# Performance work log

Hardware: AMD Instinct MI355X
Metric: run time of the kernel (lower is better)

## Reference

```python
import jax, jax.numpy as jnp
import numpy as np
from jax import lax

P_COARSE, P_FINE = 8, 4
EMBED_DIM = 128


def _patchify(x, p):
    # torch unfold(kernel=p, stride=p) then transpose: [B, Hp*Wp, C*p*p]
    B, C, H, W = x.shape
    Hp, Wp = H // p, W // p
    t = x.reshape(B, C, Hp, p, Wp, p).transpose(0, 2, 4, 1, 3, 5)
    return t.reshape(B, Hp * Wp, C * p * p), Hp, Wp


def _edge_map(x):
    gray = x.mean(axis=1, keepdims=True)
    kx = jnp.array([[-1., 0., 1.], [-2., 0., 2.], [-1., 0., 1.]], gray.dtype)[None, None]
    ky = jnp.array([[-1., -2., -1.], [0., 0., 0.], [1., 2., 1.]], gray.dtype)[None, None]
    pad = [(1, 1), (1, 1)]
    sx = lax.conv_general_dilated(gray, kx, (1, 1), pad)
    sy = lax.conv_general_dilated(gray, ky, (1, 1), pad)
    e = jnp.sqrt(sx * sx + sy * sy)
    B, _, H, W = e.shape
    # avg_pool2d(4, stride=4)
    return e.reshape(B, 1, H // 4, 4, W // 4, 4).mean(axis=(3, 5))


def _compact(tok, m):
    # stream-compact masked rows to the front, zero-pad the rest (pad_sequence semantics, padded to full Nf)
    Nf, D = tok.shape
    pos = jnp.cumsum(m) - 1
    pos = jnp.where(m, pos, Nf)  # unmasked rows go to overflow slot
    out = jnp.zeros((Nf + 1, D), tok.dtype).at[pos].set(tok)
    return out[:Nf]


def setup_inputs() -> dict:
    key = jax.random.key(0)
    ks = jax.random.split(key, 6)
    D = EMBED_DIM
    pd_c = 1 * P_COARSE * P_COARSE
    pd_f = 1 * P_FINE * P_FINE
    return {
        "x": jax.random.normal(ks[0], (8, 1, 512, 512), jnp.float32),
        "w_coarse": jax.random.normal(ks[1], (pd_c, D), jnp.float32) / np.sqrt(pd_c),
        "b_coarse": jnp.zeros((D,), jnp.float32),
        "w_fine": jax.random.normal(ks[2], (pd_f, D), jnp.float32) / np.sqrt(pd_f),
        "b_fine": jnp.zeros((D,), jnp.float32),
        "type_emb": jax.random.normal(ks[3], (2, D), jnp.float32) * 0.02,
    }


def reference(x, w_coarse, b_coarse, w_fine, b_fine, type_emb):
    B = x.shape[0]
    # coarse branch
    pc, Hc, Wc = _patchify(x, P_COARSE)
    coarse = pc @ w_coarse + b_coarse + type_emb[0]  # [B, Nc, D]
    # edge-driven mask
    edges = _edge_map(x)  # [B,1,He,We]
    mask = edges > edges.mean(axis=(2, 3), keepdims=True)
    # fine branch
    pf, Hf, Wf = _patchify(x, P_FINE)
    fine = pf @ w_fine + b_fine  # [B, Nf, D]
    # nearest upsample mask to (Hf, Wf): integer factor repeat
    m = mask[:, 0]
    m = jnp.repeat(jnp.repeat(m, Hf // m.shape[1], axis=1), Wf // m.shape[2], axis=2)
    mask_flat = m.reshape(B, -1)  # [B, Nf]
    fine_c = jax.vmap(_compact)(fine, mask_flat) + type_emb[1]
    tokens = jnp.concatenate([coarse, fine_c], axis=1)
    return tokens, mask_flat
```

## Files before the change

### kernel.cpp

```cpp
#include <hip/hip_runtime.h>

#define IMH 512
#define IMW 512
#define BATCH 8
#define NTOK 20480
#define NC 4096
#define NF 16384
#define ED 128

__global__ __launch_bounds__(256) void k_edge(const float* __restrict__ x,
                                              double* __restrict__ edges,
                                              double* __restrict__ tsum) {
    __shared__ float esm[66][68];
    __shared__ double dred[4];
    int blk = blockIdx.x;
    int t = threadIdx.x;
    int lane = t & 63, wid = t >> 6;
    int b = blk >> 6;
    int tile = blk & 63;
    int ty0 = (tile >> 3) * 64;
    int tx0 = (tile & 7) * 64;
    const float* img = x + (size_t)b * (IMH * IMW);
    for (int idx = t; idx < 66 * 66; idx += 256) {
        int r = idx / 66, c = idx - r * 66;
        int gy = ty0 - 1 + r, gx = tx0 - 1 + c;
        float v = 0.f;
        if (gy >= 0 && gy < IMH && gx >= 0 && gx < IMW) v = img[gy * IMW + gx];
        esm[r][c] = v;
    }
    __syncthreads();
    int cy = t >> 4, cx = t & 15;
    double acc = 0.0;
    #pragma unroll
    for (int dy = 0; dy < 4; ++dy) {
        int py = cy * 4 + dy + 1;
        #pragma unroll
        for (int dx = 0; dx < 4; ++dx) {
            int px = cx * 4 + dx + 1;
            double a00 = (double)esm[py - 1][px - 1];
            double a01 = (double)esm[py - 1][px];
            double a02 = (double)esm[py - 1][px + 1];
            double a10 = (double)esm[py][px - 1];
            double a12 = (double)esm[py][px + 1];
            double a20 = (double)esm[py + 1][px - 1];
            double a21 = (double)esm[py + 1][px];
            double a22 = (double)esm[py + 1][px + 1];
            double sx = (a02 + 2.0 * a12 + a22) - (a00 + 2.0 * a10 + a20);
            double sy = (a20 + 2.0 * a21 + a22) - (a00 + 2.0 * a01 + a02);
            acc += sqrt(sx * sx + sy * sy);
        }
    }
    double cell = acc * (1.0 / 16.0);
    int gy = (ty0 >> 2) + cy;
    int gx = (tx0 >> 2) + cx;
    edges[((size_t)b << 14) + gy * 128 + gx] = cell;
    double sc = cell;
    #pragma unroll
    for (int off = 32; off > 0; off >>= 1) sc += __shfl_xor(sc, off);
    if (lane == 0) dred[wid] = sc;
    __syncthreads();
    if (t == 0) tsum[b * 64 + tile] = dred[0] + dred[1] + dred[2] + dred[3];
}

__global__ __launch_bounds__(1024) void k_scan(const double* __restrict__ edges,
                                               const double* __restrict__ tsum,
                                               int* __restrict__ pos,
                                               int* __restrict__ Karr,
                                               float* __restrict__ mask_out) {
    int b = blockIdx.x;
    int t = threadIdx.x;
    int lane = t & 63, wid = t >> 6;
    __shared__ int wcnt[16];
    const double* ts = tsum + b * 64;
    double total = 0.0;
    #pragma unroll
    for (int j = 0; j < 64; ++j) total += ts[j];
    double mean = total * (1.0 / 16384.0);

    const double* e = edges + ((size_t)b << 14);
    double v[16];
    #pragma unroll
    for (int j = 0; j < 8; ++j) {
        double2 dv = *(const double2*)&e[t * 16 + j * 2];
        v[2 * j] = dv.x; v[2 * j + 1] = dv.y;
    }
    int m[16], cnt = 0;
    #pragma unroll
    for (int j = 0; j < 16; ++j) { m[j] = (v[j] > mean) ? 1 : 0; cnt += m[j]; }
    int incl = cnt;
    #pragma unroll
    for (int off = 1; off < 64; off <<= 1) {
        int up = __shfl_up(incl, off);
        if (lane >= off) incl += up;
    }
    if (lane == 63) wcnt[wid] = incl;
    __syncthreads();
    int woff = 0, Ktot = 0;
    #pragma unroll
    for (int w = 0; w < 16; ++w) { int c = wcnt[w]; Ktot += c; if (w < wid) woff += c; }
    int run = woff + incl - cnt;
    float mf[16]; int pv[16];
    #pragma unroll
    for (int j = 0; j < 16; ++j) {
        pv[j] = m[j] ? run : -1;
        run += m[j];
        mf[j] = m[j] ? 1.0f : 0.0f;
    }
    float* mb = mask_out + ((size_t)b << 14) + t * 16;
    int* pb = pos + ((size_t)b << 14) + t * 16;
    #pragma unroll
    for (int q = 0; q < 4; ++q) {
        *(float4*)&mb[q * 4] = make_float4(mf[4 * q], mf[4 * q + 1], mf[4 * q + 2], mf[4 * q + 3]);
        *(int4*)&pb[q * 4] = make_int4(pv[4 * q], pv[4 * q + 1], pv[4 * q + 2], pv[4 * q + 3]);
    }
    if (t == 0) Karr[b] = Ktot;
}

__global__ __launch_bounds__(256) void k_mega(const float* __restrict__ x,
                                              const float* __restrict__ wc,
                                              const float* __restrict__ bc,
                                              const float* __restrict__ wfp,
                                              const float* __restrict__ bfp,
                                              const float* __restrict__ temb,
                                              const int* __restrict__ pos,
                                              const int* __restrict__ Karr,
                                              float* __restrict__ out) {
    __shared__ float smx[4][256];
    int blk = blockIdx.x;
    int t = threadIdx.x;
    int lane = t & 63;
    int b = blk >> 7;
    int r128 = blk & 127;

    {
        int pblk = r128 * 32;
        int wv = __builtin_amdgcn_readfirstlane(t >> 6);
        int h = wv & 1;
        int p0 = pblk + (wv >> 1) * 16;
        int d = h * 64 + lane;
        float wcol[64];
        #pragma unroll
        for (int k = 0; k < 64; ++k) wcol[k] = wc[k * ED + d];
        float base = bc[d] + temb[d];
        const float* img = x + ((size_t)b * IMH + (p0 >> 6) * 8) * IMW + (p0 & 63) * 8;
        float* dst = out + ((size_t)b * NTOK + p0) * ED + d;
        #pragma unroll
        for (int p = 0; p < 16; ++p) {
            const float* pimg = img + p * 8;
            float acc = base;
            #pragma unroll
            for (int r = 0; r < 8; ++r) {
                const float* rp = pimg + r * IMW;
                acc += rp[0] * wcol[r * 8 + 0] + rp[1] * wcol[r * 8 + 1]
                     + rp[2] * wcol[r * 8 + 2] + rp[3] * wcol[r * 8 + 3]
                     + rp[4] * wcol[r * 8 + 4] + rp[5] * wcol[r * 8 + 5]
                     + rp[6] * wcol[r * 8 + 6] + rp[7] * wcol[r * 8 + 7];
            }
            dst[(size_t)p * ED] = acc;
        }
    }
    asm volatile("" ::: "memory");

    int d4 = t & 31;
    int g = t >> 5;
    float4 wcol[16];
    #pragma unroll
    for (int k = 0; k < 16; ++k) wcol[k] = *(const float4*)&wfp[k * ED + d4 * 4];
    float4 fill = *(const float4*)&temb[ED + d4 * 4];
    float4 bse = *(const float4*)&bfp[d4 * 4];
    float4 fbase = make_float4(bse.x + fill.x, bse.y + fill.y, bse.z + fill.z, bse.w + fill.w);
    int K = Karr[b];
    const int* posb = pos + ((size_t)b << 14);
    float* tok = out + ((size_t)b * NTOK + NC) * ED;

    #pragma unroll
    for (int u = 0; u < 2; ++u) {
        int i0 = (r128 * 2 + u) * 64;
        int hf = i0 >> 7;
        int wf0 = i0 & 127;
        const float* img = x + ((size_t)b * IMH + hf * 4) * IMW + wf0 * 4;
        __syncthreads();
        {
            int r = t >> 6, c4 = t & 63;
            *(float4*)&smx[r][c4 * 4] = *(const float4*)&img[r * IMW + c4 * 4];
        }
        __syncthreads();
        #pragma unroll
        for (int pp = 0; pp < 8; ++pp) {
            int p = g + pp * 8;
            int i = i0 + p;
            int ps = posb[i];
            if (ps >= 0) {
                float4 acc = fbase;
                #pragma unroll
                for (int r = 0; r < 4; ++r) {
                    float4 vv = *(const float4*)&smx[r][p * 4];
                    acc.x += vv.x * wcol[4 * r].x + vv.y * wcol[4 * r + 1].x + vv.z * wcol[4 * r + 2].x + vv.w * wcol[4 * r + 3].x;
                    acc.y += vv.x * wcol[4 * r].y + vv.y * wcol[4 * r + 1].y + vv.z * wcol[4 * r + 2].y + vv.w * wcol[4 * r + 3].y;
                    acc.z += vv.x * wcol[4 * r].z + vv.y * wcol[4 * r + 1].z + vv.z * wcol[4 * r + 2].z + vv.w * wcol[4 * r + 3].z;
                    acc.w += vv.x * wcol[4 * r].w + vv.y * wcol[4 * r + 1].w + vv.z * wcol[4 * r + 2].w + vv.w * wcol[4 * r + 3].w;
                }
                *(float4*)(tok + ((size_t)ps * 32 + d4) * 4) = acc;
            }
            if (i >= K) {
                *(float4*)(tok + ((size_t)i * 32 + d4) * 4) = fill;
            }
        }
    }
}

extern "C" void kernel_launch(void* const* d_in, const int* in_sizes, int n_in,
                              void* d_out, int out_size, void* d_ws, size_t ws_size,
                              hipStream_t stream) {
    const float* x    = (const float*)d_in[0];
    const float* wc   = (const float*)d_in[1];
    const float* bc   = (const float*)d_in[2];
    const float* wfp  = (const float*)d_in[3];
    const float* bfp  = (const float*)d_in[4];
    const float* temb = (const float*)d_in[5];
    float* out = (float*)d_out;

    char* wsb = (char*)d_ws;
    double* edges = (double*)wsb;
    double* tsum  = (double*)(wsb + (size_t)BATCH * NF * 8);
    int* pos  = (int*)(wsb + (size_t)BATCH * NF * 8 + 4096);
    int* Karr = (int*)(wsb + (size_t)BATCH * NF * 8 + 4096 + (size_t)BATCH * NF * 4);
    float* mask_out = out + (size_t)BATCH * NTOK * ED;

    k_edge<<<dim3(512), 256, 0, stream>>>(x, edges, tsum);
    k_scan<<<dim3(BATCH), 1024, 0, stream>>>(edges, tsum, pos, Karr, mask_out);
    k_mega<<<dim3(1024), 256, 0, stream>>>(x, wc, bc, wfp, bfp, temb, pos, Karr, out);
}
```

Before: 54.68 us.

## Move coarse projection into edge kernel and restructure fine projection kernel

The coarse patch projection moves out of the final kernel and into the edge-map kernel as extra blocks. It no longer depends on the mask, so it can run before the serial scan instead of after it. The fine projection becomes its own kernel: each thread computes one output column for 16 patches and reads pixels straight from global memory instead of staging them in shared memory. This shortens the critical path after the scan, at the cost of uncoalesced-looking scalar image reads and a larger first kernel.

```diff
diff --git a/kernel.cpp b/kernel.cpp
--- a/kernel.cpp
+++ b/kernel.cpp
@@ -8,132 +8,21 @@
 #define NF 16384
 #define ED 128
 
-__global__ __launch_bounds__(256) void k_edge(const float* __restrict__ x,
-                                              double* __restrict__ edges,
-                                              double* __restrict__ tsum) {
+__global__ __launch_bounds__(256) void k1_edge_coarse(const float* __restrict__ x,
+                                                      const float* __restrict__ wc,
+                                                      const float* __restrict__ bc,
+                                                      const float* __restrict__ temb,
+                                                      float* __restrict__ out,
+                                                      double* __restrict__ edges,
+                                                      double* __restrict__ tsum) {
     __shared__ float esm[66][68];
     __shared__ double dred[4];
     int blk = blockIdx.x;
     int t = threadIdx.x;
     int lane = t & 63, wid = t >> 6;
-    int b = blk >> 6;
-    int tile = blk & 63;
-    int ty0 = (tile >> 3) * 64;
-    int tx0 = (tile & 7) * 64;
-    const float* img = x + (size_t)b * (IMH * IMW);
-    for (int idx = t; idx < 66 * 66; idx += 256) {
-        int r = idx / 66, c = idx - r * 66;
-        int gy = ty0 - 1 + r, gx = tx0 - 1 + c;
-        float v = 0.f;
-        if (gy >= 0 && gy < IMH && gx >= 0 && gx < IMW) v = img[gy * IMW + gx];
-        esm[r][c] = v;
-    }
-    __syncthreads();
-    int cy = t >> 4, cx = t & 15;
-    double acc = 0.0;
-    #pragma unroll
-    for (int dy = 0; dy < 4; ++dy) {
-        int py = cy * 4 + dy + 1;
-        #pragma unroll
-        for (int dx = 0; dx < 4; ++dx) {
-            int px = cx * 4 + dx + 1;
-            double a00 = (double)esm[py - 1][px - 1];
-            double a01 = (double)esm[py - 1][px];
-            double a02 = (double)esm[py - 1][px + 1];
-            double a10 = (double)esm[py][px - 1];
-            double a12 = (double)esm[py][px + 1];
-            double a20 = (double)esm[py + 1][px - 1];
-            double a21 = (double)esm[py + 1][px];
-            double a22 = (double)esm[py + 1][px + 1];
-            double sx = (a02 + 2.0 * a12 + a22) - (a00 + 2.0 * a10 + a20);
-            double sy = (a20 + 2.0 * a21 + a22) - (a00 + 2.0 * a01 + a02);
-            acc += sqrt(sx * sx + sy * sy);
-        }
-    }
-    double cell = acc * (1.0 / 16.0);
-    int gy = (ty0 >> 2) + cy;
-    int gx = (tx0 >> 2) + cx;
-    edges[((size_t)b << 14) + gy * 128 + gx] = cell;
-    double sc = cell;
-    #pragma unroll
-    for (int off = 32; off > 0; off >>= 1) sc += __shfl_xor(sc, off);
-    if (lane == 0) dred[wid] = sc;
-    __syncthreads();
-    if (t == 0) tsum[b * 64 + tile] = dred[0] + dred[1] + dred[2] + dred[3];
-}
-
-__global__ __launch_bounds__(1024) void k_scan(const double* __restrict__ edges,
-                                               const double* __restrict__ tsum,
-                                               int* __restrict__ pos,
-                                               int* __restrict__ Karr,
-                                               float* __restrict__ mask_out) {
-    int b = blockIdx.x;
-    int t = threadIdx.x;
-    int lane = t & 63, wid = t >> 6;
-    __shared__ int wcnt[16];
-    const double* ts = tsum + b * 64;
-    double total = 0.0;
-    #pragma unroll
-    for (int j = 0; j < 64; ++j) total += ts[j];
-    double mean = total * (1.0 / 16384.0);
-
-    const double* e = edges + ((size_t)b << 14);
-    double v[16];
-    #pragma unroll
-    for (int j = 0; j < 8; ++j) {
-        double2 dv = *(const double2*)&e[t * 16 + j * 2];
-        v[2 * j] = dv.x; v[2 * j + 1] = dv.y;
-    }
-    int m[16], cnt = 0;
-    #pragma unroll
-    for (int j = 0; j < 16; ++j) { m[j] = (v[j] > mean) ? 1 : 0; cnt += m[j]; }
-    int incl = cnt;
-    #pragma unroll
-    for (int off = 1; off < 64; off <<= 1) {
-        int up = __shfl_up(incl, off);
-        if (lane >= off) incl += up;
-    }
-    if (lane == 63) wcnt[wid] = incl;
-    __syncthreads();
-    int woff = 0, Ktot = 0;
-    #pragma unroll
-    for (int w = 0; w < 16; ++w) { int c = wcnt[w]; Ktot += c; if (w < wid) woff += c; }
-    int run = woff + incl - cnt;
-    float mf[16]; int pv[16];
-    #pragma unroll
-    for (int j = 0; j < 16; ++j) {
-        pv[j] = m[j] ? run : -1;
-        run += m[j];
-        mf[j] = m[j] ? 1.0f : 0.0f;
-    }
-    float* mb = mask_out + ((size_t)b << 14) + t * 16;
-    int* pb = pos + ((size_t)b << 14) + t * 16;
-    #pragma unroll
-    for (int q = 0; q < 4; ++q) {
-        *(float4*)&mb[q * 4] = make_float4(mf[4 * q], mf[4 * q + 1], mf[4 * q + 2], mf[4 * q + 3]);
-        *(int4*)&pb[q * 4] = make_int4(pv[4 * q], pv[4 * q + 1], pv[4 * q + 2], pv[4 * q + 3]);
-    }
-    if (t == 0) Karr[b] = Ktot;
-}
-
-__global__ __launch_bounds__(256) void k_mega(const float* __restrict__ x,
-                                              const float* __restrict__ wc,
-                                              const float* __restrict__ bc,
-                                              const float* __restrict__ wfp,
-                                              const float* __restrict__ bfp,
-                                              const float* __restrict__ temb,
-                                              const int* __restrict__ pos,
-                                              const int* __restrict__ Karr,
-                                              float* __restrict__ out) {
-    __shared__ float smx[4][256];
-    int blk = blockIdx.x;
-    int t = threadIdx.x;
-    int lane = t & 63;
-    int b = blk >> 7;
-    int r128 = blk & 127;
-
-    {
-        int pblk = r128 * 32;
+    if (blk < 1024) {
+        int b = blk >> 7;
+        int pblk = (blk & 127) * 32;
         int wv = __builtin_amdgcn_readfirstlane(t >> 6);
         int h = wv & 1;
         int p0 = pblk + (wv >> 1) * 16;
@@ -158,53 +47,151 @@
             }
             dst[(size_t)p * ED] = acc;
         }
-    }
-    asm volatile("" ::: "memory");
-
-    int d4 = t & 31;
-    int g = t >> 5;
-    float4 wcol[16];
-    #pragma unroll
-    for (int k = 0; k < 16; ++k) wcol[k] = *(const float4*)&wfp[k * ED + d4 * 4];
-    float4 fill = *(const float4*)&temb[ED + d4 * 4];
-    float4 bse = *(const float4*)&bfp[d4 * 4];
-    float4 fbase = make_float4(bse.x + fill.x, bse.y + fill.y, bse.z + fill.z, bse.w + fill.w);
+    } else {
+        int blk2 = blk - 1024;
+        int b = blk2 >> 6;
+        int tile = blk2 & 63;
+        int ty0 = (tile >> 3) * 64;
+        int tx0 = (tile & 7) * 64;
+        const float* img = x + (size_t)b * (IMH * IMW);
+        for (int idx = t; idx < 66 * 66; idx += 256) {
+            int r = idx / 66, c = idx - r * 66;
+            int gy = ty0 - 1 + r, gx = tx0 - 1 + c;
+            float v = 0.f;
+            if (gy >= 0 && gy < IMH && gx >= 0 && gx < IMW) v = img[gy * IMW + gx];
+            esm[r][c] = v;
+        }
+        __syncthreads();
+        int cy = t >> 4, cx = t & 15;
+        double acc = 0.0;
+        #pragma unroll
+        for (int dy = 0; dy < 4; ++dy) {
+            int py = cy * 4 + dy + 1;
+            #pragma unroll
+            for (int dx = 0; dx < 4; ++dx) {
+                int px = cx * 4 + dx + 1;
+                double a00 = (double)esm[py - 1][px - 1];
+                double a01 = (double)esm[py - 1][px];
+                double a02 = (double)esm[py - 1][px + 1];
+                double a10 = (double)esm[py][px - 1];
+                double a12 = (double)esm[py][px + 1];
+                double a20 = (double)esm[py + 1][px - 1];
+                double a21 = (double)esm[py + 1][px];
+                double a22 = (double)esm[py + 1][px + 1];
+                double sx = (a02 + 2.0 * a12 + a22) - (a00 + 2.0 * a10 + a20);
+                double sy = (a20 + 2.0 * a21 + a22) - (a00 + 2.0 * a01 + a02);
+                acc += sqrt(sx * sx + sy * sy);
+            }
+        }
+        double cell = acc * (1.0 / 16.0);
+        int gy = (ty0 >> 2) + cy;
+        int gx = (tx0 >> 2) + cx;
+        edges[((size_t)b << 14) + gy * 128 + gx] = cell;
+        double sc = cell;
+        #pragma unroll
+        for (int off = 32; off > 0; off >>= 1) sc += __shfl_xor(sc, off);
+        if (lane == 0) dred[wid] = sc;
+        __syncthreads();
+        if (t == 0) tsum[b * 64 + tile] = dred[0] + dred[1] + dred[2] + dred[3];
+    }
+}
+
+__global__ __launch_bounds__(1024) void k_scan(const double* __restrict__ edges,
+                                               const double* __restrict__ tsum,
+                                               int* __restrict__ pos,
+                                               int* __restrict__ Karr,
+                                               float* __restrict__ mask_out) {
+    int b = blockIdx.x;
+    int t = threadIdx.x;
+    int lane = t & 63, wid = t >> 6;
+    __shared__ int wcnt[16];
+    const double* ts = tsum + b * 64;
+    double total = 0.0;
+    #pragma unroll
+    for (int j = 0; j < 64; ++j) total += ts[j];
+    double mean = total * (1.0 / 16384.0);
+
+    const double* e = edges + ((size_t)b << 14);
+    double v[16];
+    #pragma unroll
+    for (int j = 0; j < 8; ++j) {
+        double2 dv = *(const double2*)&e[t * 16 + j * 2];
+        v[2 * j] = dv.x; v[2 * j + 1] = dv.y;
+    }
+    int m[16], cnt = 0;
+    #pragma unroll
+    for (int j = 0; j < 16; ++j) { m[j] = (v[j] > mean) ? 1 : 0; cnt += m[j]; }
+    int incl = cnt;
+    #pragma unroll
+    for (int off = 1; off < 64; off <<= 1) {
+        int up = __shfl_up(incl, off);
+        if (lane >= off) incl += up;
+    }
+    if (lane == 63) wcnt[wid] = incl;
+    __syncthreads();
+    int woff = 0, Ktot = 0;
+    #pragma unroll
+    for (int w = 0; w < 16; ++w) { int c = wcnt[w]; Ktot += c; if (w < wid) woff += c; }
+    int run = woff + incl - cnt;
+    float mf[16]; int pv[16];
+    #pragma unroll
+    for (int j = 0; j < 16; ++j) {
+        pv[j] = m[j] ? run : -1;
+        run += m[j];
+        mf[j] = m[j] ? 1.0f : 0.0f;
+    }
+    float* mb = mask_out + ((size_t)b << 14) + t * 16;
+    int* pb = pos + ((size_t)b << 14) + t * 16;
+    #pragma unroll
+    for (int q = 0; q < 4; ++q) {
+        *(float4*)&mb[q * 4] = make_float4(mf[4 * q], mf[4 * q + 1], mf[4 * q + 2], mf[4 * q + 3]);
+        *(int4*)&pb[q * 4] = make_int4(pv[4 * q], pv[4 * q + 1], pv[4 * q + 2], pv[4 * q + 3]);
+    }
+    if (t == 0) Karr[b] = Ktot;
+}
+
+__global__ __launch_bounds__(256) void k_fine(const float* __restrict__ x,
+                                              const float* __restrict__ wfp,
+                                              const float* __restrict__ bfp,
+                                              const float* __restrict__ temb,
+                                              const int* __restrict__ pos,
+                                              const int* __restrict__ Karr,
+                                              float* __restrict__ out) {
+    int b = blockIdx.y;
+    int t = threadIdx.x;
+    int lane = t & 63;
+    int wv = __builtin_amdgcn_readfirstlane(t >> 6);
+    int h = wv & 1;
+    int p0 = blockIdx.x * 32 + (wv >> 1) * 16;
+    int d = h * 64 + lane;
+    float wcol[16];
+    #pragma unroll
+    for (int k = 0; k < 16; ++k) wcol[k] = wfp[k * ED + d];
+    float fill = temb[ED + d];
+    float fbase = bfp[d] + fill;
     int K = Karr[b];
     const int* posb = pos + ((size_t)b << 14);
+    int hf = p0 >> 7;
+    int wf0 = p0 & 127;
+    const float* img = x + ((size_t)b * IMH + hf * 4) * IMW + wf0 * 4;
     float* tok = out + ((size_t)b * NTOK + NC) * ED;
-
-    #pragma unroll
-    for (int u = 0; u < 2; ++u) {
-        int i0 = (r128 * 2 + u) * 64;
-        int hf = i0 >> 7;
-        int wf0 = i0 & 127;
-        const float* img = x + ((size_t)b * IMH + hf * 4) * IMW + wf0 * 4;
-        __syncthreads();
-        {
-            int r = t >> 6, c4 = t & 63;
-            *(float4*)&smx[r][c4 * 4] = *(const float4*)&img[r * IMW + c4 * 4];
-        }
-        __syncthreads();
-        #pragma unroll
-        for (int pp = 0; pp < 8; ++pp) {
-            int p = g + pp * 8;
-            int i = i0 + p;
-            int ps = posb[i];
-            if (ps >= 0) {
-                float4 acc = fbase;
-                #pragma unroll
-                for (int r = 0; r < 4; ++r) {
-                    float4 vv = *(const float4*)&smx[r][p * 4];
-                    acc.x += vv.x * wcol[4 * r].x + vv.y * wcol[4 * r + 1].x + vv.z * wcol[4 * r + 2].x + vv.w * wcol[4 * r + 3].x;
-                    acc.y += vv.x * wcol[4 * r].y + vv.y * wcol[4 * r + 1].y + vv.z * wcol[4 * r + 2].y + vv.w * wcol[4 * r + 3].y;
-                    acc.z += vv.x * wcol[4 * r].z + vv.y * wcol[4 * r + 1].z + vv.z * wcol[4 * r + 2].z + vv.w * wcol[4 * r + 3].z;
-                    acc.w += vv.x * wcol[4 * r].w + vv.y * wcol[4 * r + 1].w + vv.z * wcol[4 * r + 2].w + vv.w * wcol[4 * r + 3].w;
-                }
-                *(float4*)(tok + ((size_t)ps * 32 + d4) * 4) = acc;
-            }
-            if (i >= K) {
-                *(float4*)(tok + ((size_t)i * 32 + d4) * 4) = fill;
-            }
+    #pragma unroll
+    for (int p = 0; p < 16; ++p) {
+        int i = p0 + p;
+        int ps = posb[i];
+        const float* pimg = img + p * 4;
+        float acc = fbase;
+        #pragma unroll
+        for (int r = 0; r < 4; ++r) {
+            const float* rp = pimg + r * IMW;
+            acc += rp[0] * wcol[4 * r + 0] + rp[1] * wcol[4 * r + 1]
+                 + rp[2] * wcol[4 * r + 2] + rp[3] * wcol[4 * r + 3];
+        }
+        if (ps >= 0) {
+            tok[(size_t)ps * ED + d] = acc;
+        }
+        if (i >= K) {
+            tok[(size_t)i * ED + d] = fill;
         }
     }
 }
@@ -227,7 +214,7 @@
     int* Karr = (int*)(wsb + (size_t)BATCH * NF * 8 + 4096 + (size_t)BATCH * NF * 4);
     float* mask_out = out + (size_t)BATCH * NTOK * ED;
 
-    k_edge<<<dim3(512), 256, 0, stream>>>(x, edges, tsum);
+    k1_edge_coarse<<<dim3(1536), 256, 0, stream>>>(x, wc, bc, temb, out, edges, tsum);
     k_scan<<<dim3(BATCH), 1024, 0, stream>>>(edges, tsum, pos, Karr, mask_out);
-    k_mega<<<dim3(1024), 256, 0, stream>>>(x, wc, bc, wfp, bfp, temb, pos, Karr, out);
-}
+    k_fine<<<dim3(512, BATCH), 256, 0, stream>>>(x, wfp, bfp, temb, pos, Karr, out);
+}
```

Measured after the change: 61.36 us. 1.12x slower.
